# Kernel optimization log

Measured on AMD Instinct MI355X. Metric: run time of the kernel, lower is better.

## Reference

```python
import jax, jax.numpy as jnp
import numpy as np

HEAD_DIM = 256
ROTARY_DIM = 128  # max(2, int(0.5*256) rounded down to even)
HALF_ROT = ROTARY_DIM // 2   # 64
HALF_HEAD = HEAD_DIM // 2    # 128
WAVELENGTH = 10000.0
ROPE_SCALING = 1.0
SOFT_CAP = 50.0
EPS = 1e-6
NQ = 8
NKV = 4
GROUPS = NQ // NKV
NEG_INF = -1e9


def rms_norm(x, scale):
    # keras-hub Gemma RMSNorm: fp32 compute, out = x * rsqrt(mean(x^2)+eps) * (1+scale)
    x32 = x.astype(jnp.float32)
    var = jnp.mean(jnp.square(x32), axis=-1, keepdims=True)
    y = x32 * jax.lax.rsqrt(var + EPS)
    return (y * (1.0 + scale.astype(jnp.float32))).astype(x.dtype)


def l2_norm(x):
    # Gemma4VNorm: pure L2 normalization over head_dim, no learned scale
    x32 = x.astype(jnp.float32)
    ss = jnp.sum(jnp.square(x32), axis=-1, keepdims=True)
    return (x32 * jax.lax.rsqrt(ss + EPS)).astype(x.dtype)


def apply_partial_rope(x):
    # x: [B, S, N, HEAD_DIM]. Partial proportional rotation: only the first
    # HALF_ROT elements of each HALF_HEAD half get rotated. RoPE inverse freqs
    # use denominator_dim = HEAD_DIM (not rotary_dim).
    S = x.shape[1]
    inv_freq = 1.0 / (WAVELENGTH ** (jnp.arange(0, ROTARY_DIM, 2, dtype=jnp.float32) / HEAD_DIM))  # [HALF_ROT]
    pos = jnp.arange(S, dtype=jnp.float32) / ROPE_SCALING
    freq = pos[:, None] * inv_freq[None, :]             # [S, HALF_ROT]
    cos = jnp.cos(freq)[None, :, None, :].astype(x.dtype)
    sin = jnp.sin(freq)[None, :, None, :].astype(x.dtype)
    x1 = x[..., :HALF_HEAD]
    x2 = x[..., HALF_HEAD:]
    x1r, x1n = x1[..., :HALF_ROT], x1[..., HALF_ROT:]
    x2r, x2n = x2[..., :HALF_ROT], x2[..., HALF_ROT:]
    # rotate-half form: [x1r, x2r]*cos + [-x2r, x1r]*sin
    y1r = x1r * cos - x2r * sin
    y2r = x2r * cos + x1r * sin
    return jnp.concatenate([y1r, x1n, y2r, x2n], axis=-1)


def setup_inputs() -> dict:
    key = jax.random.key(0)
    ks = jax.random.split(key, 6)
    B, S, D = 2, 2048, 2048
    x = jax.random.normal(ks[0], (B, S, D), jnp.float32)
    # causal mask [B, S, S]
    attention_mask = jnp.broadcast_to(jnp.tril(jnp.ones((S, S), bool))[None], (B, S, S))
    w_scale = 0.02
    Wq = jax.random.normal(ks[1], (NQ, D, HEAD_DIM), jnp.float32) * w_scale
    Wk = jax.random.normal(ks[2], (NKV, D, HEAD_DIM), jnp.float32) * w_scale
    Wv = jax.random.normal(ks[3], (NKV, D, HEAD_DIM), jnp.float32) * w_scale
    Wo = jax.random.normal(ks[4], (NQ, HEAD_DIM, D), jnp.float32) * w_scale
    q_scale = jnp.zeros((HEAD_DIM,), jnp.float32)
    k_scale = jnp.zeros((HEAD_DIM,), jnp.float32)
    return {"x": x, "attention_mask": attention_mask, "Wq": Wq, "Wk": Wk,
            "Wv": Wv, "Wo": Wo, "q_scale": q_scale, "k_scale": k_scale}


def reference(x, attention_mask, Wq, Wk, Wv, Wo, q_scale, k_scale):
    B, S, D = x.shape
    q = jnp.einsum('btd,ndh->btnh', x, Wq)
    q = apply_partial_rope(rms_norm(q, q_scale))
    k = jnp.einsum('bsd,kdh->bskh', x, Wk)
    k = apply_partial_rope(rms_norm(k, k_scale))
    v = l2_norm(jnp.einsum('bsd,kdh->bskh', x, Wv))
    # grouped-query attention, scaling = 1.0 (Gemma4 relies on QK norm)
    qg = q.reshape(B, S, NKV, GROUPS, HEAD_DIM)
    logits = jnp.einsum('btkgh,bskh->bkgts', qg, k)
    # logit soft cap
    logits = jnp.tanh(logits / SOFT_CAP) * SOFT_CAP
    mask = attention_mask[:, None, None, :, :]
    logits = jnp.where(mask, logits, NEG_INF)
    probs = jax.nn.softmax(logits.astype(jnp.float32), axis=-1).astype(logits.dtype)
    out = jnp.einsum('bkgts,bskh->btkgh', probs, v).reshape(B, S, NQ, HEAD_DIM)
    return jnp.einsum('btnh,nhd->btd', out, Wo)
```

## Files before the change

kernel.cpp:

```cpp
#include <hip/hip_runtime.h>

#define AS1 __attribute__((address_space(1)))
#define AS3 __attribute__((address_space(3)))

typedef __attribute__((ext_vector_type(8))) _Float16 f16x8;
typedef __attribute__((ext_vector_type(4))) _Float16 f16x4;
typedef __attribute__((ext_vector_type(4))) float f32x4;

#define MFMA_K16(a, b, c) __builtin_amdgcn_mfma_f32_16x16x16f16(a, b, c, 0, 0, 0)
#define MFMA_K32(a, b, c) __builtin_amdgcn_mfma_f32_16x16x32_f16(a, b, c, 0, 0, 0)

__device__ __forceinline__ unsigned short f2h(float f) {
    union { _Float16 h; unsigned short u; } v; v.h = (_Float16)f; return v.u;
}

__device__ __forceinline__ void gload16(const void* g, void* l) {
    __builtin_amdgcn_global_load_lds((const AS1 unsigned int*)g, (AS3 unsigned int*)l, 16, 0, 0);
}

#define GBAR() __builtin_amdgcn_s_barrier()
#define VM4()  asm volatile("s_waitcnt vmcnt(4)" ::: "memory")
#define VM0()  asm volatile("s_waitcnt vmcnt(0)" ::: "memory")

__global__ __launch_bounds__(256) void k_prep(const float* __restrict__ x,
                                              const float* __restrict__ Wq,
                                              const float* __restrict__ Wk,
                                              const float* __restrict__ Wv,
                                              const float* __restrict__ Wo,
                                              unsigned short* __restrict__ xh,
                                              unsigned short* __restrict__ WT,
                                              unsigned short* __restrict__ WoT) {
    int z = blockIdx.z;
    if (z == 24) {
        int blk = blockIdx.y * 8 + blockIdx.x;
        int t = threadIdx.y * 32 + threadIdx.x;
        const float4* s4 = (const float4*)x;
        ushort4* d4 = (ushort4*)xh;
        int base = blk * 4096 + t;
#pragma unroll
        for (int i = 0; i < 16; i++) {
            float4 v = s4[base + i * 256];
            ushort4 u;
            u.x = f2h(v.x); u.y = f2h(v.y); u.z = f2h(v.z); u.w = f2h(v.w);
            d4[base + i * 256] = u;
        }
        return;
    }
    const float* src; unsigned short* dst;
    int ld_src, c0, r0;
    if (z < 16) {
        if (z < 8)       { src = Wq + (size_t)z * 524288;        dst = WT + (size_t)z * 524288; }
        else if (z < 12) { src = Wk + (size_t)(z - 8) * 524288;  dst = WT + (size_t)2048 * 2048 + (size_t)(z - 8) * 524288; }
        else             { src = Wv + (size_t)(z - 12) * 524288; dst = WT + (size_t)3072 * 2048 + (size_t)(z - 12) * 524288; }
        ld_src = 256;
        c0 = blockIdx.x * 32; r0 = blockIdx.y * 32;
    } else {
        src = Wo; dst = WoT; ld_src = 2048;
        c0 = ((z - 16) * 8 + blockIdx.x) * 32; r0 = blockIdx.y * 32;
    }
    __shared__ float tile[32][33];
    int tx = threadIdx.x, ty = threadIdx.y;
#pragma unroll
    for (int i = 0; i < 4; i++)
        tile[ty + i * 8][tx] = src[(size_t)(r0 + ty + i * 8) * ld_src + c0 + tx];
    __syncthreads();
#pragma unroll
    for (int i = 0; i < 4; i++)
        dst[(size_t)(c0 + ty + i * 8) * 2048 + r0 + tx] = f2h(tile[tx][ty + i * 8]);
}

__global__ __launch_bounds__(256) void k_vtrans(const float* __restrict__ qkv,
                                                unsigned short* __restrict__ Vt) {
    __shared__ float tile[32][33];
    int z = blockIdx.z;
    int b = z >> 2, h = z & 3;
    const float* src = qkv + (size_t)b * 8388608 + 3072 + h * 256;
    unsigned short* dst = Vt + (size_t)z * 524288;
    int c0 = blockIdx.x * 32, r0 = blockIdx.y * 32;
    int tx = threadIdx.x, ty = threadIdx.y;
#pragma unroll
    for (int i = 0; i < 4; i++)
        tile[ty + i * 8][tx] = src[(size_t)(r0 + ty + i * 8) * 4096 + c0 + tx];
    __syncthreads();
#pragma unroll
    for (int i = 0; i < 4; i++)
        dst[(size_t)(c0 + ty + i * 8) * 2048 + r0 + tx] = f2h(tile[tx][ty + i * 8]);
}

template<int BUF, int MIH>
__device__ __forceinline__ void rdA(const unsigned short* SA, int wm, int fr, int g,
                                    f16x8 (&af)[4][2]) {
#pragma unroll
    for (int m = 0; m < 4; m++)
#pragma unroll
        for (int kk = 0; kk < 2; kk++) {
            int pos = wm * 64 + m * 16 + fr;
            af[m][kk] = *(const f16x8*)(SA + BUF * 16384 + MIH * 8192 + pos * 64 +
                                        (((kk * 4 + g) ^ (fr & 7)) << 3));
        }
}

template<int BUF, int NIH>
__device__ __forceinline__ void rdB(const unsigned short* SB, int wn, int fr, int g,
                                    f16x8 (&bf)[2][2]) {
#pragma unroll
    for (int ni2 = 0; ni2 < 2; ni2++)
#pragma unroll
        for (int kk = 0; kk < 2; kk++) {
            int pos = wn * 32 + ni2 * 16 + fr;
            bf[ni2][kk] = *(const f16x8*)(SB + BUF * 16384 + NIH * 8192 + pos * 64 +
                                          (((kk * 4 + g) ^ (fr & 7)) << 3));
        }
}

template<int MIH, int NIH>
__device__ __forceinline__ void mm16(f16x8 (&af)[4][2], f16x8 (&bf)[2][2], f32x4 (&acc)[8][4]) {
    __builtin_amdgcn_s_setprio(1);
#pragma unroll
    for (int m = 0; m < 4; m++)
#pragma unroll
        for (int ni2 = 0; ni2 < 2; ni2++)
#pragma unroll
            for (int kk = 0; kk < 2; kk++)
                acc[MIH * 4 + m][NIH * 2 + ni2] = MFMA_K32(af[m][kk], bf[ni2][kk],
                                                           acc[MIH * 4 + m][NIH * 2 + ni2]);
    __builtin_amdgcn_s_setprio(0);
}

__global__ __launch_bounds__(512, 1) void k_gemm256(const unsigned short* __restrict__ A,
                                                    const unsigned short* __restrict__ Bt,
                                                    float* __restrict__ C,
                                                    int M, int N, int K, int nbx) {
    __shared__ __align__(16) unsigned short sm[65536];
    unsigned short* SA = sm;
    unsigned short* SB = sm + 32768;

    int tid = threadIdx.x, lane = tid & 63, wid = tid >> 6;
    int g = lane >> 4, fr = lane & 15;
    int wm = wid >> 2, wn = wid & 3;

    int bid = blockIdx.x;
    int sid = (bid & 7) * ((int)gridDim.x >> 3) + (bid >> 3);
    int by = sid / nbx, bx = sid % nbx;
    int rowA0 = by * 256, colB0 = bx * 256;

    f32x4 acc[8][4];
#pragma unroll
    for (int mi = 0; mi < 8; mi++)
#pragma unroll
        for (int ni = 0; ni < 4; ni++) acc[mi][ni] = (f32x4){0.f, 0.f, 0.f, 0.f};

    auto stA = [&](int buf, int h, int kt) {
#pragma unroll
        for (int t = 0; t < 2; t++) {
            int i = t * 512 + tid;
            int pos = i >> 3;
            int grow = rowA0 + ((pos >> 6) << 7) + h * 64 + (pos & 63);
            int cg = (i & 7) ^ (pos & 7);
            gload16(A + (size_t)grow * K + kt * 64 + cg * 8,
                    SA + buf * 16384 + h * 8192 + pos * 64 + (i & 7) * 8);
        }
    };
    auto stB = [&](int buf, int h, int kt) {
#pragma unroll
        for (int t = 0; t < 2; t++) {
            int i = t * 512 + tid;
            int pos = i >> 3;
            int gcol = colB0 + ((pos >> 5) << 6) + h * 32 + (pos & 31);
            int cg = (i & 7) ^ (pos & 7);
            gload16(Bt + (size_t)gcol * K + kt * 64 + cg * 8,
                    SB + buf * 16384 + h * 8192 + pos * 64 + (i & 7) * 8);
        }
    };

    int nT = K >> 6;
    stA(0, 0, 0); stB(0, 0, 0); stA(0, 1, 0); stB(0, 1, 0);
    stA(1, 0, 1); stB(1, 0, 1);
    VM4();
    GBAR();

    f16x8 af[4][2], bf[2][2];
    int nIt = nT >> 1;
    for (int it = 0; it < nIt; it++) {
        int T = it * 2;
        bool s36 = (T + 2 < nT), s78 = (T + 3 < nT);
        rdA<0, 0>(SA, wm, fr, g, af); rdB<0, 0>(SB, wn, fr, g, bf);
        stA(1, 1, T + 1);
        GBAR(); mm16<0, 0>(af, bf, acc); GBAR();
        rdB<0, 1>(SB, wn, fr, g, bf);
        stB(1, 1, T + 1);
        GBAR(); mm16<0, 1>(af, bf, acc); GBAR();
        rdA<0, 1>(SA, wm, fr, g, af); rdB<0, 0>(SB, wn, fr, g, bf);
        if (s36) stA(0, 0, T + 2);
        GBAR(); mm16<1, 0>(af, bf, acc); GBAR();
        rdB<0, 1>(SB, wn, fr, g, bf);
        if (s36) { stB(0, 0, T + 2); VM4(); } else { VM0(); }
        GBAR(); mm16<1, 1>(af, bf, acc); GBAR();
        rdA<1, 0>(SA, wm, fr, g, af); rdB<1, 0>(SB, wn, fr, g, bf);
        if (s36) stA(0, 1, T + 2);
        GBAR(); mm16<0, 0>(af, bf, acc); GBAR();
        rdB<1, 1>(SB, wn, fr, g, bf);
        if (s36) stB(0, 1, T + 2);
        GBAR(); mm16<0, 1>(af, bf, acc); GBAR();
        rdA<1, 1>(SA, wm, fr, g, af); rdB<1, 0>(SB, wn, fr, g, bf);
        if (s78) stA(1, 0, T + 3);
        GBAR(); mm16<1, 0>(af, bf, acc); GBAR();
        rdB<1, 1>(SB, wn, fr, g, bf);
        if (s78) { stB(1, 0, T + 3); VM4(); } else { VM0(); }
        GBAR(); mm16<1, 1>(af, bf, acc); GBAR();
    }

#pragma unroll
    for (int mi = 0; mi < 8; mi++) {
        int row = rowA0 + wm * 128 + mi * 16 + g * 4;
#pragma unroll
        for (int ni = 0; ni < 4; ni++) {
            int col = colB0 + wn * 64 + ni * 16 + fr;
#pragma unroll
            for (int r = 0; r < 4; r++)
                C[(size_t)(row + r) * N + col] = acc[mi][ni][r];
        }
    }
}

__global__ __launch_bounds__(256) void k_gemm_f16(const unsigned short* __restrict__ A,
                                                  const unsigned short* __restrict__ Bt,
                                                  float* __restrict__ C,
                                                  int M, int N, int K) {
    __shared__ unsigned short As[128 * 64];
    __shared__ unsigned short Bs[128 * 64];
    int tid = threadIdx.x;
    int lane = tid & 63, wid = tid >> 6;
    int g = lane >> 4, fr = lane & 15;
    int rowA0 = blockIdx.y * 128;
    int colB0 = blockIdx.x * 128;

    f32x4 zero = {0.f, 0.f, 0.f, 0.f};
    f32x4 acc[4][4];
#pragma unroll
    for (int mi = 0; mi < 4; mi++)
#pragma unroll
        for (int ni = 0; ni < 4; ni++) acc[mi][ni] = zero;

    const unsigned short* ag[4];
    const unsigned short* bg[4];
#pragma unroll
    for (int j = 0; j < 4; j++) {
        int id = j * 256 + tid;
        int r = id >> 3;
        int c = (id & 7) ^ (r & 7);
        ag[j] = A + (size_t)(rowA0 + r) * K + c * 8;
        bg[j] = Bt + (size_t)(colB0 + r) * K + c * 8;
    }

    int nK = K >> 6;
    for (int kt = 0; kt < nK; kt++) {
#pragma unroll
        for (int j = 0; j < 4; j++) {
            int id = j * 256 + tid;
            gload16(ag[j], As + id * 8);
            gload16(bg[j], Bs + id * 8);
            ag[j] += 64; bg[j] += 64;
        }
        __syncthreads();
#pragma unroll
        for (int kk = 0; kk < 2; kk++) {
            f16x8 af[4], bfr[4];
#pragma unroll
            for (int mi = 0; mi < 4; mi++) {
                int r = (wid >> 1) * 64 + mi * 16 + fr;
                af[mi] = *(const f16x8*)(As + r * 64 + ((((kk << 2) + g) ^ (r & 7)) << 3));
            }
#pragma unroll
            for (int ni = 0; ni < 4; ni++) {
                int r = (wid & 1) * 64 + ni * 16 + fr;
                bfr[ni] = *(const f16x8*)(Bs + r * 64 + ((((kk << 2) + g) ^ (r & 7)) << 3));
            }
#pragma unroll
            for (int mi = 0; mi < 4; mi++)
#pragma unroll
                for (int ni = 0; ni < 4; ni++)
                    acc[mi][ni] = MFMA_K32(af[mi], bfr[ni], acc[mi][ni]);
        }
        __syncthreads();
    }

#pragma unroll
    for (int mi = 0; mi < 4; mi++) {
        int row = rowA0 + (wid >> 1) * 64 + mi * 16 + g * 4;
#pragma unroll
        for (int ni = 0; ni < 4; ni++) {
            int col = colB0 + (wid & 1) * 64 + ni * 16 + fr;
#pragma unroll
            for (int r = 0; r < 4; r++)
                C[(size_t)(row + r) * N + col] = acc[mi][ni][r];
        }
    }
}

__global__ __launch_bounds__(256) void k_norm_rope(float* __restrict__ qkv,
                                                   const float* __restrict__ q_scale,
                                                   const float* __restrict__ k_scale,
                                                   unsigned short* __restrict__ Qh,
                                                   unsigned short* __restrict__ Kh) {
    __shared__ float Y[256];
    __shared__ float red[4];
    int blk = blockIdx.x;
    int bt = blk >> 4, slot = blk & 15;
    int b = bt >> 11, t = bt & 2047;
    int h = threadIdx.x;
    int lane = h & 63, wid = h >> 6;

    float x = qkv[(size_t)bt * 4096 + slot * 256 + h];
    float v = x * x;
#pragma unroll
    for (int m = 1; m < 64; m <<= 1) v += __shfl_xor(v, m);
    if (lane == 0) red[wid] = v;
    __syncthreads();
    float ss = red[0] + red[1] + red[2] + red[3];

    float y;
    if (slot < 12) {
        float fac = rsqrtf(ss * (1.0f / 256.0f) + 1e-6f);
        const float* sc = (slot < 8) ? q_scale : k_scale;
        y = x * fac * (1.0f + sc[h]);
    } else {
        float fac = rsqrtf(ss + 1e-6f);
        y = x * fac;
    }
    Y[h] = y;
    __syncthreads();

    if (slot < 12) {
        float out;
        int hm = h & 127;
        if (hm < 64) {
            float inv = exp2f(-(float)hm * 0.10381025296522993f);
            float fr = (float)t * inv;
            float s = sinf(fr), c = cosf(fr);
            float y1 = Y[hm], y2 = Y[128 + hm];
            out = (h < 128) ? (y1 * c - y2 * s) : (y2 * c + y1 * s);
        } else {
            out = y;
        }
        unsigned short hv = f2h(out);
        if (slot < 8)
            Qh[((size_t)(b * 8 + slot) * 2048 + t) * 256 + h] = hv;
        else
            Kh[((size_t)(b * 4 + (slot - 8)) * 2048 + t) * 256 + h] = hv;
    } else {
        qkv[(size_t)bt * 4096 + slot * 256 + h] = y;
    }
}

__global__ __launch_bounds__(512, 2) void k_attn(const unsigned short* __restrict__ Qhg,
                                                 const unsigned short* __restrict__ Khg,
                                                 const unsigned short* __restrict__ Vtg,
                                                 unsigned short* __restrict__ attn) {
    __shared__ __align__(16) char smem[132096];
    unsigned short* Ks = (unsigned short*)smem;
    unsigned short* Vs = (unsigned short*)(smem + 65536);
    float* ML = (float*)(smem + 131072);
    float* X = (float*)smem;

    int id = blockIdx.x;
    int bkv = id & 7;
    int npar = (id >> 3) & 1;
    int pair = id >> 4;
    int b = bkv >> 2, kv = bkv & 3;
    int n = kv * 2 + npar;
    int bn = b * 8 + n;

    int tid = threadIdx.x, lane = tid & 63, wid = tid >> 6;
    int g = lane >> 4, fr = lane & 15;
    int r2 = wid & 3, c2 = wid >> 2;
    int g4 = g * 4;

    const unsigned short* Kh = Khg + (size_t)bkv * 2048 * 256;
    const unsigned short* Vh = Vtg + (size_t)bkv * 256 * 2048;
    const unsigned short* Qb = Qhg + (size_t)bn * 2048 * 256;

    const unsigned short* kb[4];
    const unsigned short* vb[4];
    int sdst[4];
#pragma unroll
    for (int t2 = 0; t2 < 4; t2++) {
        int c_ = t2 * 512 + tid;
        int r = c_ >> 5, c = (c_ & 31) ^ (r & 7);
        kb[t2] = Kh + (size_t)r * 256 + c * 8;
        int d = c_ >> 3, cv = (c_ & 7) ^ (d & 7);
        vb[t2] = Vh + (size_t)d * 2048 + cv * 8;
        sdst[t2] = c_ * 8;
    }

    int krbase[2];
#pragma unroll
    for (int t16 = 0; t16 < 2; t16++) krbase[t16] = (c2 * 32 + t16 * 16 + fr) * 256;
    int s7 = fr & 7;
    int vslot[2];
#pragma unroll
    for (int t16 = 0; t16 < 2; t16++) vslot[t16] = (((c2 * 4 + t16 * 2 + (g >> 1)) ^ s7) << 3) + (g & 1) * 4;

    for (int half = 0; half < 2; half++) {
        int j = half ? 31 - pair : pair;
        int q0 = j * 64 + r2 * 16;

        const unsigned short* qrow = Qb + (size_t)(q0 + fr) * 256;
        f16x8 aq[8];
#pragma unroll
        for (int kk = 0; kk < 8; kk++) aq[kk] = *(const f16x8*)(qrow + kk * 32 + g * 8);

        f32x4 zero4 = {0.f, 0.f, 0.f, 0.f};
        f32x4 o[16];
#pragma unroll
        for (int i2 = 0; i2 < 16; i2++) o[i2] = zero4;
        float m_run = -1e30f;
        float l_run = 0.f;

        auto STAGE = [&](int bufi, int kt2) {
#pragma unroll
            for (int t2 = 0; t2 < 4; t2++) {
                gload16(kb[t2] + (size_t)kt2 * 16384, Ks + bufi * 16384 + sdst[t2]);
                gload16(vb[t2] + kt2 * 64, Vs + bufi * 16384 + sdst[t2]);
            }
        };

        STAGE(0, 0);
        __syncthreads();

        for (int kt = 0; kt <= j; kt++) {
            int cur = kt & 1;
            if (kt < j) STAGE(cur ^ 1, kt + 1);

            const unsigned short* KH = Ks + cur * 16384;
            const unsigned short* VC = Vs + cur * 16384;
            int k0 = kt * 64;

            f32x4 se[2] = {zero4, zero4}, so2[2] = {zero4, zero4};
            __builtin_amdgcn_s_setprio(1);
#pragma unroll
            for (int kk = 0; kk < 8; kk += 2) {
#pragma unroll
                for (int t16 = 0; t16 < 2; t16++) {
                    f16x8 bk0 = *(const f16x8*)(KH + krbase[t16] + ((((kk << 2) + g) ^ s7) << 3));
                    f16x8 bk1 = *(const f16x8*)(KH + krbase[t16] + (((((kk + 1) << 2) + g) ^ s7) << 3));
                    se[t16] = MFMA_K32(bk0, aq[kk], se[t16]);
                    so2[t16] = MFMA_K32(bk1, aq[kk + 1], so2[t16]);
                }
            }
            __builtin_amdgcn_s_setprio(0);

            int qg = q0 + fr;
            float pv[2][4];
            float ml = -1e30f;
#pragma unroll
            for (int t16 = 0; t16 < 2; t16++)
#pragma unroll
                for (int r = 0; r < 4; r++) {
                    float s = se[t16][r] + so2[t16][r];
                    float e = __expf(0.04f * s);
                    s = 50.f - 100.f * __builtin_amdgcn_rcpf(1.f + e);
                    int key = k0 + c2 * 32 + t16 * 16 + g4 + r;
                    if (key > qg) s = -1e9f;
                    pv[t16][r] = s;
                    ml = fmaxf(ml, s);
                }
            ml = fmaxf(ml, __shfl_xor(ml, 16));
            ml = fmaxf(ml, __shfl_xor(ml, 32));

            if (__any(ml > m_run + 8.f)) {
                float mnew = fmaxf(m_run, ml);
                float swl = __expf(m_run - mnew);
                m_run = mnew;
                l_run *= swl;
                float swr[4];
#pragma unroll
                for (int r = 0; r < 4; r++) swr[r] = __shfl(swl, g4 + r);
#pragma unroll
                for (int nt = 0; nt < 16; nt++)
#pragma unroll
                    for (int r = 0; r < 4; r++) o[nt][r] *= swr[r];
            }

            f16x4 pf[2];
#pragma unroll
            for (int t16 = 0; t16 < 2; t16++)
#pragma unroll
                for (int r = 0; r < 4; r++) {
                    float p = __expf(pv[t16][r] - m_run);
                    l_run += p;
                    pf[t16][r] = (_Float16)p;
                }

            __builtin_amdgcn_s_setprio(1);
#pragma unroll
            for (int nt = 0; nt < 16; nt++) {
                int dbase = (nt * 16 + fr) * 64;
                f16x4 bv0 = *(const f16x4*)(VC + dbase + vslot[0]);
                f16x4 bv1 = *(const f16x4*)(VC + dbase + vslot[1]);
                o[nt] = MFMA_K16(pf[0], bv0, o[nt]);
                o[nt] = MFMA_K16(pf[1], bv1, o[nt]);
            }
            __builtin_amdgcn_s_setprio(0);
            __syncthreads();
        }

        float l2 = l_run + __shfl_xor(l_run, 16);
        l2 += __shfl_xor(l2, 32);
        if (lane < 16) {
            float* mlw = ML + ((c2 * 4 + r2) * 16 + lane) * 2;
            mlw[0] = m_run; mlw[1] = l2;
        }
        __syncthreads();
        float wO[4], li[4];
#pragma unroll
        for (int r = 0; r < 4; r++) {
            int qq = g4 + r;
            const float* p0 = ML + (r2 * 16 + qq) * 2;
            const float* p1 = ML + ((4 + r2) * 16 + qq) * 2;
            float m0 = p0[0], l0 = p0[1], m1 = p1[0], l1 = p1[1];
            float ms = fmaxf(m0, m1);
            float w0 = __expf(m0 - ms), w1 = __expf(m1 - ms);
            li[r] = __builtin_amdgcn_rcpf(fmaxf(l0 * w0 + l1 * w1, 1e-30f));
            wO[r] = c2 ? w1 : w0;
        }
        float* Xl = X + (r2 * 64 + lane) * 68;
        if (c2 == 1) {
#pragma unroll
            for (int nt = 0; nt < 16; nt++)
#pragma unroll
                for (int r = 0; r < 4; r++) Xl[nt * 4 + r] = o[nt][r] * wO[r];
        }
        __syncthreads();
        if (c2 == 0) {
#pragma unroll
            for (int nt = 0; nt < 16; nt++)
#pragma unroll
                for (int r = 0; r < 4; r++) {
                    float val = (o[nt][r] * wO[r] + Xl[nt * 4 + r]) * li[r];
                    int qr = q0 + g4 + r;
                    attn[(size_t)(b * 2048 + qr) * 2048 + n * 256 + nt * 16 + fr] = f2h(val);
                }
        }
        __syncthreads();
    }
}

extern "C" void kernel_launch(void* const* d_in, const int* in_sizes, int n_in,
                              void* d_out, int out_size, void* d_ws, size_t ws_size,
                              hipStream_t stream) {
    const float* x       = (const float*)d_in[0];
    const float* Wq      = (const float*)d_in[2];
    const float* Wk      = (const float*)d_in[3];
    const float* Wv      = (const float*)d_in[4];
    const float* Wo      = (const float*)d_in[5];
    const float* q_scale = (const float*)d_in[6];
    const float* k_scale = (const float*)d_in[7];
    float* out = (float*)d_out;
    char* ws = (char*)d_ws;

    const size_t MB = 1024 * 1024;
    unsigned short* xh    = (unsigned short*)ws;
    unsigned short* Qh    = (unsigned short*)ws;
    unsigned short* WT    = (unsigned short*)(ws + 16 * MB);
    unsigned short* Kh    = (unsigned short*)(ws + 16 * MB);
    unsigned short* Vt    = (unsigned short*)(ws + 24 * MB);
    unsigned short* WoT   = (unsigned short*)(ws + 32 * MB);
    float*          qkv   = (float*)(ws + 40 * MB);
    unsigned short* attnb = (unsigned short*)(ws + 40 * MB);

    dim3 tb(32, 8);
    k_prep<<<dim3(8, 64, 25), tb, 0, stream>>>(x, Wq, Wk, Wv, Wo, xh, WT, WoT);

    k_gemm256<<<dim3(256), dim3(512), 0, stream>>>(xh, WT, qkv, 4096, 4096, 2048, 16);
    k_norm_rope<<<dim3(65536), dim3(256), 0, stream>>>(qkv, q_scale, k_scale, Qh, Kh);
    k_vtrans<<<dim3(8, 64, 8), tb, 0, stream>>>(qkv, Vt);
    k_attn<<<dim3(256), dim3(512), 0, stream>>>(Qh, Kh, Vt, attnb);

    k_gemm_f16<<<dim3(16, 32), dim3(256), 0, stream>>>(attnb, WoT, out, 4096, 2048, 2048);
}
```

Before: 269.4 us.

## Fuse RMS/L2 norm, partial RoPE and V transpose into QKV GEMM epilogue

The QKV projection GEMM no longer writes an fp32 qkv buffer. Its epilogue computes per-row sum of squares across waves through shared memory, applies RMS or L2 normalisation, applies RoPE by exchanging the paired halves through LDS, and writes fp16 Q/K directly, or transposes V through a swizzled LDS tile into Vt. This drops the separate norm/rope and V-transpose kernels and the fp32 round trip of roughly 64MB through global memory. In exchange the epilogue is longer, adds barriers and extra LDS traffic, and issues scattered 2-byte stores for Q/K.

```diff
diff --git a/kernel.cpp b/kernel.cpp
--- a/kernel.cpp
+++ b/kernel.cpp
@@ -69,68 +69,14 @@
         dst[(size_t)(c0 + ty + i * 8) * 2048 + r0 + tx] = f2h(tile[tx][ty + i * 8]);
 }
 
-__global__ __launch_bounds__(256) void k_vtrans(const float* __restrict__ qkv,
-                                                unsigned short* __restrict__ Vt) {
-    __shared__ float tile[32][33];
-    int z = blockIdx.z;
-    int b = z >> 2, h = z & 3;
-    const float* src = qkv + (size_t)b * 8388608 + 3072 + h * 256;
-    unsigned short* dst = Vt + (size_t)z * 524288;
-    int c0 = blockIdx.x * 32, r0 = blockIdx.y * 32;
-    int tx = threadIdx.x, ty = threadIdx.y;
-#pragma unroll
-    for (int i = 0; i < 4; i++)
-        tile[ty + i * 8][tx] = src[(size_t)(r0 + ty + i * 8) * 4096 + c0 + tx];
-    __syncthreads();
-#pragma unroll
-    for (int i = 0; i < 4; i++)
-        dst[(size_t)(c0 + ty + i * 8) * 2048 + r0 + tx] = f2h(tile[tx][ty + i * 8]);
-}
-
-template<int BUF, int MIH>
-__device__ __forceinline__ void rdA(const unsigned short* SA, int wm, int fr, int g,
-                                    f16x8 (&af)[4][2]) {
-#pragma unroll
-    for (int m = 0; m < 4; m++)
-#pragma unroll
-        for (int kk = 0; kk < 2; kk++) {
-            int pos = wm * 64 + m * 16 + fr;
-            af[m][kk] = *(const f16x8*)(SA + BUF * 16384 + MIH * 8192 + pos * 64 +
-                                        (((kk * 4 + g) ^ (fr & 7)) << 3));
-        }
-}
-
-template<int BUF, int NIH>
-__device__ __forceinline__ void rdB(const unsigned short* SB, int wn, int fr, int g,
-                                    f16x8 (&bf)[2][2]) {
-#pragma unroll
-    for (int ni2 = 0; ni2 < 2; ni2++)
-#pragma unroll
-        for (int kk = 0; kk < 2; kk++) {
-            int pos = wn * 32 + ni2 * 16 + fr;
-            bf[ni2][kk] = *(const f16x8*)(SB + BUF * 16384 + NIH * 8192 + pos * 64 +
-                                          (((kk * 4 + g) ^ (fr & 7)) << 3));
-        }
-}
-
-template<int MIH, int NIH>
-__device__ __forceinline__ void mm16(f16x8 (&af)[4][2], f16x8 (&bf)[2][2], f32x4 (&acc)[8][4]) {
-    __builtin_amdgcn_s_setprio(1);
-#pragma unroll
-    for (int m = 0; m < 4; m++)
-#pragma unroll
-        for (int ni2 = 0; ni2 < 2; ni2++)
-#pragma unroll
-            for (int kk = 0; kk < 2; kk++)
-                acc[MIH * 4 + m][NIH * 2 + ni2] = MFMA_K32(af[m][kk], bf[ni2][kk],
-                                                           acc[MIH * 4 + m][NIH * 2 + ni2]);
-    __builtin_amdgcn_s_setprio(0);
-}
-
-__global__ __launch_bounds__(512, 1) void k_gemm256(const unsigned short* __restrict__ A,
-                                                    const unsigned short* __restrict__ Bt,
-                                                    float* __restrict__ C,
-                                                    int M, int N, int K, int nbx) {
+__global__ __launch_bounds__(512, 1) void k_gemm_qkv(const unsigned short* __restrict__ A,
+                                                     const unsigned short* __restrict__ Bt,
+                                                     const float* __restrict__ q_scale,
+                                                     const float* __restrict__ k_scale,
+                                                     unsigned short* __restrict__ Qh,
+                                                     unsigned short* __restrict__ Kh,
+                                                     unsigned short* __restrict__ Vt,
+                                                     int K, int nbx) {
     __shared__ __align__(16) unsigned short sm[65536];
     unsigned short* SA = sm;
     unsigned short* SB = sm + 32768;
@@ -142,7 +88,7 @@
     int bid = blockIdx.x;
     int sid = (bid & 7) * ((int)gridDim.x >> 3) + (bid >> 3);
     int by = sid / nbx, bx = sid % nbx;
-    int rowA0 = by * 256, colB0 = bx * 256;
+    int rowA0 = by * 256;
 
     f32x4 acc[8][4];
 #pragma unroll
@@ -166,11 +112,44 @@
         for (int t = 0; t < 2; t++) {
             int i = t * 512 + tid;
             int pos = i >> 3;
-            int gcol = colB0 + ((pos >> 5) << 6) + h * 32 + (pos & 31);
+            int gcol = bx * 256 + ((pos >> 5) << 6) + h * 32 + (pos & 31);
             int cg = (i & 7) ^ (pos & 7);
             gload16(Bt + (size_t)gcol * K + kt * 64 + cg * 8,
                     SB + buf * 16384 + h * 8192 + pos * 64 + (i & 7) * 8);
         }
+    };
+
+    auto rdA2 = [&](int buf, int mih, f16x8 (&af)[4][2]) {
+#pragma unroll
+        for (int m = 0; m < 4; m++)
+#pragma unroll
+            for (int kk = 0; kk < 2; kk++) {
+                int pos = wm * 64 + m * 16 + fr;
+                af[m][kk] = *(const f16x8*)(SA + buf * 16384 + mih * 8192 + pos * 64 +
+                                            (((kk * 4 + g) ^ (fr & 7)) << 3));
+            }
+    };
+    auto rdB2 = [&](int buf, int nih, f16x8 (&bf)[2][2]) {
+#pragma unroll
+        for (int ni2 = 0; ni2 < 2; ni2++)
+#pragma unroll
+            for (int kk = 0; kk < 2; kk++) {
+                int pos = wn * 32 + ni2 * 16 + fr;
+                bf[ni2][kk] = *(const f16x8*)(SB + buf * 16384 + nih * 8192 + pos * 64 +
+                                              (((kk * 4 + g) ^ (fr & 7)) << 3));
+            }
+    };
+    auto mm = [&](int mih, int nih, f16x8 (&af)[4][2], f16x8 (&bf)[2][2]) {
+        __builtin_amdgcn_s_setprio(1);
+#pragma unroll
+        for (int m = 0; m < 4; m++)
+#pragma unroll
+            for (int ni2 = 0; ni2 < 2; ni2++)
+#pragma unroll
+                for (int kk = 0; kk < 2; kk++)
+                    acc[mih * 4 + m][nih * 2 + ni2] = MFMA_K32(af[m][kk], bf[ni2][kk],
+                                                               acc[mih * 4 + m][nih * 2 + ni2]);
+        __builtin_amdgcn_s_setprio(0);
     };
 
     int nT = K >> 6;
@@ -184,42 +163,152 @@
     for (int it = 0; it < nIt; it++) {
         int T = it * 2;
         bool s36 = (T + 2 < nT), s78 = (T + 3 < nT);
-        rdA<0, 0>(SA, wm, fr, g, af); rdB<0, 0>(SB, wn, fr, g, bf);
+        rdA2(0, 0, af); rdB2(0, 0, bf);
         stA(1, 1, T + 1);
-        GBAR(); mm16<0, 0>(af, bf, acc); GBAR();
-        rdB<0, 1>(SB, wn, fr, g, bf);
+        GBAR(); mm(0, 0, af, bf); GBAR();
+        rdB2(0, 1, bf);
         stB(1, 1, T + 1);
-        GBAR(); mm16<0, 1>(af, bf, acc); GBAR();
-        rdA<0, 1>(SA, wm, fr, g, af); rdB<0, 0>(SB, wn, fr, g, bf);
+        GBAR(); mm(0, 1, af, bf); GBAR();
+        rdA2(0, 1, af); rdB2(0, 0, bf);
         if (s36) stA(0, 0, T + 2);
-        GBAR(); mm16<1, 0>(af, bf, acc); GBAR();
-        rdB<0, 1>(SB, wn, fr, g, bf);
+        GBAR(); mm(1, 0, af, bf); GBAR();
+        rdB2(0, 1, bf);
         if (s36) { stB(0, 0, T + 2); VM4(); } else { VM0(); }
-        GBAR(); mm16<1, 1>(af, bf, acc); GBAR();
-        rdA<1, 0>(SA, wm, fr, g, af); rdB<1, 0>(SB, wn, fr, g, bf);
+        GBAR(); mm(1, 1, af, bf); GBAR();
+        rdA2(1, 0, af); rdB2(1, 0, bf);
         if (s36) stA(0, 1, T + 2);
-        GBAR(); mm16<0, 0>(af, bf, acc); GBAR();
-        rdB<1, 1>(SB, wn, fr, g, bf);
+        GBAR(); mm(0, 0, af, bf); GBAR();
+        rdB2(1, 1, bf);
         if (s36) stB(0, 1, T + 2);
-        GBAR(); mm16<0, 1>(af, bf, acc); GBAR();
-        rdA<1, 1>(SA, wm, fr, g, af); rdB<1, 0>(SB, wn, fr, g, bf);
+        GBAR(); mm(0, 1, af, bf); GBAR();
+        rdA2(1, 1, af); rdB2(1, 0, bf);
         if (s78) stA(1, 0, T + 3);
-        GBAR(); mm16<1, 0>(af, bf, acc); GBAR();
-        rdB<1, 1>(SB, wn, fr, g, bf);
+        GBAR(); mm(1, 0, af, bf); GBAR();
+        rdB2(1, 1, bf);
         if (s78) { stB(1, 0, T + 3); VM4(); } else { VM0(); }
-        GBAR(); mm16<1, 1>(af, bf, acc); GBAR();
-    }
-
-#pragma unroll
-    for (int mi = 0; mi < 8; mi++) {
-        int row = rowA0 + wm * 128 + mi * 16 + g * 4;
-#pragma unroll
-        for (int ni = 0; ni < 4; ni++) {
-            int col = colB0 + wn * 64 + ni * 16 + fr;
+        GBAR(); mm(1, 1, af, bf); GBAR();
+    }
+
+    int b = by >> 3;
+    int tb = (by & 7) * 256;
+    bool isV = (bx >= 12);
+
+    float* SS = (float*)sm;
+    float ssp[8][4];
+#pragma unroll
+    for (int mi = 0; mi < 8; mi++)
+#pragma unroll
+        for (int r = 0; r < 4; r++) {
+            float s = 0.f;
+#pragma unroll
+            for (int ni = 0; ni < 4; ni++) { float v = acc[mi][ni][r]; s += v * v; }
+#pragma unroll
+            for (int m2 = 1; m2 < 16; m2 <<= 1) s += __shfl_xor(s, m2);
+            ssp[mi][r] = s;
+        }
+    if (fr == 0) {
+#pragma unroll
+        for (int mi = 0; mi < 8; mi++)
 #pragma unroll
             for (int r = 0; r < 4; r++)
-                C[(size_t)(row + r) * N + col] = acc[mi][ni][r];
-        }
+                SS[wn * 256 + wm * 128 + mi * 16 + g * 4 + r] = ssp[mi][r];
+    }
+    __syncthreads();
+
+    float sc1[4] = {1.f, 1.f, 1.f, 1.f};
+    if (!isV) {
+        const float* scp = (bx < 8) ? q_scale : k_scale;
+#pragma unroll
+        for (int ni = 0; ni < 4; ni++) sc1[ni] = 1.f + scp[wn * 64 + ni * 16 + fr];
+    }
+#pragma unroll
+    for (int mi = 0; mi < 8; mi++)
+#pragma unroll
+        for (int r = 0; r < 4; r++) {
+            int rl = wm * 128 + mi * 16 + g * 4 + r;
+            float ss = SS[rl] + SS[256 + rl] + SS[512 + rl] + SS[768 + rl];
+            float fac = isV ? rsqrtf(ss + 1e-6f) : rsqrtf(ss * (1.f / 256.f) + 1e-6f);
+#pragma unroll
+            for (int ni = 0; ni < 4; ni++) acc[mi][ni][r] *= fac * sc1[ni];
+        }
+    __syncthreads();
+
+    if (isV) {
+        unsigned short* Ysm = sm;
+#pragma unroll
+        for (int mi = 0; mi < 8; mi++)
+#pragma unroll
+            for (int r = 0; r < 4; r++) {
+                int tl = wm * 128 + mi * 16 + g * 4 + r;
+#pragma unroll
+                for (int ni = 0; ni < 4; ni++) {
+                    int d = wn * 64 + ni * 16 + fr;
+                    Ysm[tl * 256 + (d ^ ((tl & 7) << 3))] = f2h(acc[mi][ni][r]);
+                }
+            }
+        __syncthreads();
+        unsigned short* dst = Vt + (size_t)(b * 4 + (bx - 12)) * 524288;
+        int d0 = tid & 255, th = tid >> 8;
+#pragma unroll
+        for (int c = 0; c < 16; c++) {
+            int t0 = th * 128 + c * 8;
+            ushort4 w0, w1;
+            unsigned short tmp[8];
+#pragma unroll
+            for (int e = 0; e < 8; e++) {
+                int tt = t0 + e;
+                tmp[e] = Ysm[tt * 256 + (d0 ^ ((tt & 7) << 3))];
+            }
+            w0.x = tmp[0]; w0.y = tmp[1]; w0.z = tmp[2]; w0.w = tmp[3];
+            w1.x = tmp[4]; w1.y = tmp[5]; w1.z = tmp[6]; w1.w = tmp[7];
+            *(ushort4*)(dst + (size_t)d0 * 2048 + tb + t0) = w0;
+            *(ushort4*)(dst + (size_t)d0 * 2048 + tb + t0 + 4) = w1;
+        }
+    } else {
+        float* Yex = (float*)sm;
+        bool rot = !(wn & 1);
+        if (rot) {
+#pragma unroll
+            for (int mi = 0; mi < 8; mi++)
+#pragma unroll
+                for (int r = 0; r < 4; r++) {
+                    int tl = wm * 128 + mi * 16 + g * 4 + r;
+#pragma unroll
+                    for (int ni = 0; ni < 4; ni++)
+                        Yex[(wn >> 1) * 16384 + tl * 64 + ni * 16 + fr] = acc[mi][ni][r];
+                }
+        }
+        __syncthreads();
+        unsigned short* dst = (bx < 8)
+            ? Qh + (size_t)(b * 8 + bx) * 2048 * 256
+            : Kh + (size_t)(b * 4 + (bx - 8)) * 2048 * 256;
+        float invf[4];
+        if (rot) {
+#pragma unroll
+            for (int ni = 0; ni < 4; ni++)
+                invf[ni] = exp2f(-(float)(ni * 16 + fr) * 0.10381025296522993f);
+        }
+#pragma unroll
+        for (int mi = 0; mi < 8; mi++)
+#pragma unroll
+            for (int r = 0; r < 4; r++) {
+                int tl = wm * 128 + mi * 16 + g * 4 + r;
+                int t = tb + tl;
+                size_t rowoff = (size_t)t * 256 + wn * 64;
+#pragma unroll
+                for (int ni = 0; ni < 4; ni++) {
+                    float y = acc[mi][ni][r], outv;
+                    if (rot) {
+                        float pair = Yex[(1 - (wn >> 1)) * 16384 + tl * 64 + ni * 16 + fr];
+                        float ang = (float)t * invf[ni];
+                        float sn = sinf(ang), cs = cosf(ang);
+                        outv = (wn == 0) ? y * cs - pair * sn : y * cs + pair * sn;
+                    } else {
+                        outv = y;
+                    }
+                    dst[rowoff + ni * 16 + fr] = f2h(outv);
+                }
+            }
     }
 }
 
@@ -295,61 +384,6 @@
             for (int r = 0; r < 4; r++)
                 C[(size_t)(row + r) * N + col] = acc[mi][ni][r];
         }
-    }
-}
-
-__global__ __launch_bounds__(256) void k_norm_rope(float* __restrict__ qkv,
-                                                   const float* __restrict__ q_scale,
-                                                   const float* __restrict__ k_scale,
-                                                   unsigned short* __restrict__ Qh,
-                                                   unsigned short* __restrict__ Kh) {
-    __shared__ float Y[256];
-    __shared__ float red[4];
-    int blk = blockIdx.x;
-    int bt = blk >> 4, slot = blk & 15;
-    int b = bt >> 11, t = bt & 2047;
-    int h = threadIdx.x;
-    int lane = h & 63, wid = h >> 6;
-
-    float x = qkv[(size_t)bt * 4096 + slot * 256 + h];
-    float v = x * x;
-#pragma unroll
-    for (int m = 1; m < 64; m <<= 1) v += __shfl_xor(v, m);
-    if (lane == 0) red[wid] = v;
-    __syncthreads();
-    float ss = red[0] + red[1] + red[2] + red[3];
-
-    float y;
-    if (slot < 12) {
-        float fac = rsqrtf(ss * (1.0f / 256.0f) + 1e-6f);
-        const float* sc = (slot < 8) ? q_scale : k_scale;
-        y = x * fac * (1.0f + sc[h]);
-    } else {
-        float fac = rsqrtf(ss + 1e-6f);
-        y = x * fac;
-    }
-    Y[h] = y;
-    __syncthreads();
-
-    if (slot < 12) {
-        float out;
-        int hm = h & 127;
-        if (hm < 64) {
-            float inv = exp2f(-(float)hm * 0.10381025296522993f);
-            float fr = (float)t * inv;
-            float s = sinf(fr), c = cosf(fr);
-            float y1 = Y[hm], y2 = Y[128 + hm];
-            out = (h < 128) ? (y1 * c - y2 * s) : (y2 * c + y1 * s);
-        } else {
-            out = y;
-        }
-        unsigned short hv = f2h(out);
-        if (slot < 8)
-            Qh[((size_t)(b * 8 + slot) * 2048 + t) * 256 + h] = hv;
-        else
-            Kh[((size_t)(b * 4 + (slot - 8)) * 2048 + t) * 256 + h] = hv;
-    } else {
-        qkv[(size_t)bt * 4096 + slot * 256 + h] = y;
     }
 }
 
@@ -561,21 +595,16 @@
 
     const size_t MB = 1024 * 1024;
     unsigned short* xh    = (unsigned short*)ws;
-    unsigned short* Qh    = (unsigned short*)ws;
     unsigned short* WT    = (unsigned short*)(ws + 16 * MB);
-    unsigned short* Kh    = (unsigned short*)(ws + 16 * MB);
-    unsigned short* Vt    = (unsigned short*)(ws + 24 * MB);
     unsigned short* WoT   = (unsigned short*)(ws + 32 * MB);
-    float*          qkv   = (float*)(ws + 40 * MB);
-    unsigned short* attnb = (unsigned short*)(ws + 40 * MB);
+    unsigned short* Qh    = (unsigned short*)(ws + 40 * MB);
+    unsigned short* Kh    = (unsigned short*)(ws + 56 * MB);
+    unsigned short* Vt    = (unsigned short*)(ws + 64 * MB);
+    unsigned short* attnb = (unsigned short*)(ws + 72 * MB);
 
     dim3 tb(32, 8);
     k_prep<<<dim3(8, 64, 25), tb, 0, stream>>>(x, Wq, Wk, Wv, Wo, xh, WT, WoT);
-
-    k_gemm256<<<dim3(256), dim3(512), 0, stream>>>(xh, WT, qkv, 4096, 4096, 2048, 16);
-    k_norm_rope<<<dim3(65536), dim3(256), 0, stream>>>(qkv, q_scale, k_scale, Qh, Kh);
-    k_vtrans<<<dim3(8, 64, 8), tb, 0, stream>>>(qkv, Vt);
+    k_gemm_qkv<<<dim3(256), dim3(512), 0, stream>>>(xh, WT, q_scale, k_scale, Qh, Kh, Vt, 2048, 16);
     k_attn<<<dim3(256), dim3(512), 0, stream>>>(Qh, Kh, Vt, attnb);
-
     k_gemm_f16<<<dim3(16, 32), dim3(256), 0, stream>>>(attnb, WoT, out, 4096, 2048, 2048);
 }
```

Result: no change. 267.7 us (-0.6%).
